# Optimization experiments

Hardware: AMD Instinct MI355X
Metric: run time of the kernel (lower is better)

The kernel has to match this reference:

```python
import jax, jax.numpy as jnp
import numpy as np

IMG_H, IMG_W = 256, 704  # full image shape (img_metas['img_shape'])
EPS = 1e-5
B, N_CAM, D_REF, C_CH = 1, 6, 1, 256
HF, WF = 32, 88
DD = 64
BEV_H = BEV_W = 128
Q = BEV_H * BEV_W


def inverse_sigmoid(x, eps=1e-5):
    x = jnp.clip(x, 0.0, 1.0)
    return jnp.log(jnp.clip(x, eps) / jnp.clip(1.0 - x, eps))


def grid_sample_2d(feat, grid):
    # feat [N,C,H,W], grid [N,Hg,Wg,2] (x,y in [-1,1]); bilinear, zeros padding, align_corners=False
    Nn, C, H, W = feat.shape
    x = (grid[..., 0] + 1.0) * 0.5 * W - 0.5
    y = (grid[..., 1] + 1.0) * 0.5 * H - 0.5
    x0 = jnp.floor(x)
    y0 = jnp.floor(y)
    wx = x - x0
    wy = y - y0
    x0 = x0.astype(jnp.int32)
    y0 = y0.astype(jnp.int32)

    def gather(ix, iy):
        valid = (ix >= 0) & (ix < W) & (iy >= 0) & (iy < H)
        ixc = jnp.clip(ix, 0, W - 1)
        iyc = jnp.clip(iy, 0, H - 1)
        v = jax.vmap(lambda f, jx, jy: f[:, jy, jx])(feat, ixc, iyc)  # [N,C,Hg,Wg]
        return v * valid[:, None].astype(feat.dtype)

    return (gather(x0, y0) * ((1 - wx) * (1 - wy))[:, None]
            + gather(x0 + 1, y0) * (wx * (1 - wy))[:, None]
            + gather(x0, y0 + 1) * ((1 - wx) * wy)[:, None]
            + gather(x0 + 1, y0 + 1) * (wx * wy)[:, None])


def grid_sample_3d(vol, grid):
    # vol [N,C,D,H,W], grid [N,Dg,Hg,Wg,3] (x,y,z); trilinear, zeros padding, align_corners=False
    Nn, C, D, H, W = vol.shape
    x = (grid[..., 0] + 1.0) * 0.5 * W - 0.5
    y = (grid[..., 1] + 1.0) * 0.5 * H - 0.5
    z = (grid[..., 2] + 1.0) * 0.5 * D - 0.5
    x0 = jnp.floor(x); y0 = jnp.floor(y); z0 = jnp.floor(z)
    wx = x - x0; wy = y - y0; wz = z - z0
    x0 = x0.astype(jnp.int32); y0 = y0.astype(jnp.int32); z0 = z0.astype(jnp.int32)

    def gather(ix, iy, iz):
        valid = (ix >= 0) & (ix < W) & (iy >= 0) & (iy < H) & (iz >= 0) & (iz < D)
        ixc = jnp.clip(ix, 0, W - 1)
        iyc = jnp.clip(iy, 0, H - 1)
        izc = jnp.clip(iz, 0, D - 1)
        v = jax.vmap(lambda f, jx, jy, jz: f[:, jz, jy, jx])(vol, ixc, iyc, izc)
        return v * valid[:, None].astype(vol.dtype)

    return (gather(x0, y0, z0) * ((1 - wx) * (1 - wy) * (1 - wz))[:, None]
            + gather(x0 + 1, y0, z0) * (wx * (1 - wy) * (1 - wz))[:, None]
            + gather(x0, y0 + 1, z0) * ((1 - wx) * wy * (1 - wz))[:, None]
            + gather(x0 + 1, y0 + 1, z0) * (wx * wy * (1 - wz))[:, None]
            + gather(x0, y0, z0 + 1) * ((1 - wx) * (1 - wy) * wz)[:, None]
            + gather(x0 + 1, y0, z0 + 1) * (wx * (1 - wy) * wz)[:, None]
            + gather(x0, y0 + 1, z0 + 1) * ((1 - wx) * wy * wz)[:, None]
            + gather(x0 + 1, y0 + 1, z0 + 1) * (wx * wy * wz)[:, None])


def setup_inputs() -> dict:
    key = jax.random.key(0)
    ks = jax.random.split(key, 12)
    feat = jax.random.normal(ks[0], (B * N_CAM, C_CH, HF, WF), jnp.float32)
    bev_queries = jax.random.normal(ks[1], (B, Q, C_CH), jnp.float32)
    bev_pos = jax.random.normal(ks[2], (B, Q, C_CH), jnp.float32)
    reference_points = jax.random.uniform(ks[3], (B, D_REF, Q, 3), jnp.float32)
    pc_range = jnp.array([-51.2, -51.2, -5.0, 51.2, 51.2, 3.0], jnp.float32)
    # semi-realistic lidar->image projection matrices: intrinsics * axis-swap * yaw per camera
    f, cx, cy = 500.0, IMG_W / 2.0, IMG_H / 2.0
    K = np.array([[f, 0, cx, 0], [0, f, cy, 0], [0, 0, 1, 0], [0, 0, 0, 1]], np.float32)
    A = np.array([[0, -1, 0, 0], [0, 0, -1, 0], [1, 0, 0, 0], [0, 0, 0, 1]], np.float32)
    mats = []
    for i in range(N_CAM):
        th = 2.0 * np.pi * i / N_CAM
        c, s = np.cos(th), np.sin(th)
        R = np.array([[c, s, 0, 0], [-s, c, 0, 0], [0, 0, 1, 0], [0, 0, 0, 1]], np.float32)
        mats.append(K @ A @ R)
    lidar_to_img = jnp.asarray(np.stack(mats))[None]  # [1,N,4,4]
    depth_prob = jax.random.uniform(ks[4], (B * N_CAM, DD, HF, WF), jnp.float32)
    sc = 0.02
    return {
        'feat': feat, 'bev_queries': bev_queries, 'bev_pos': bev_pos,
        'reference_points': reference_points, 'pc_range': pc_range,
        'lidar_to_img': lidar_to_img, 'depth_prob': depth_prob,
        'w_pos': jax.random.normal(ks[5], (C_CH, 1), jnp.float32) * sc,
        'b_pos': jnp.zeros((1,), jnp.float32),
        'w_img': jax.random.normal(ks[6], (C_CH, N_CAM * 2), jnp.float32) * sc,
        'b_img': jnp.zeros((N_CAM * 2,), jnp.float32),
        'w_att': jax.random.normal(ks[7], (C_CH, N_CAM), jnp.float32) * sc,
        'b_att': jnp.zeros((N_CAM,), jnp.float32),
        'conv_w': jax.random.normal(ks[8], (C_CH, C_CH, 3, 3), jnp.float32) * sc,
        'conv_b': jnp.zeros((C_CH,), jnp.float32),
        'bn_gamma': jnp.ones((C_CH,), jnp.float32),
        'bn_beta': jnp.zeros((C_CH,), jnp.float32),
        'bn_mean': jnp.zeros((C_CH,), jnp.float32),
        'bn_var': jnp.ones((C_CH,), jnp.float32),
        'se_w': jax.random.normal(ks[9], (C_CH, C_CH), jnp.float32) * sc,
        'se_b': jnp.zeros((C_CH,), jnp.float32),
        'cbam_w': jax.random.normal(ks[10], (1, 2, 7, 7), jnp.float32) * 0.05,
        'cbam_b': jnp.zeros((1,), jnp.float32),
        'bev_h': BEV_H, 'bev_w': BEV_W,
    }


def reference(feat, bev_queries, bev_pos, reference_points, pc_range, lidar_to_img, depth_prob,
              w_pos, b_pos, w_img, b_img, w_att, b_att, conv_w, conv_b,
              bn_gamma, bn_beta, bn_mean, bn_var, se_w, se_b, cbam_w, cbam_b, bev_h, bev_w):
    Bq, Qn = bev_queries.shape[:2]
    D = reference_points.shape[1]
    N = lidar_to_img.shape[1]
    BN, C, Hf, Wf = feat.shape
    q = bev_queries + bev_pos
    pos_offset = q @ w_pos + b_pos  # [B,Q,1] (only_use_height)
    z = jax.nn.sigmoid(inverse_sigmoid(reference_points[..., 2:3]) + pos_offset[:, None])
    rp = jnp.concatenate([reference_points[..., :2], z], axis=-1)  # [B,D,Q,3]
    attn = (q @ w_att + b_att).reshape(Bq, 1, Qn, N, 1)
    img_off = q @ w_img + b_img  # [B,Q,2N]
    # unnormalize to lidar coords; apply_3d_transformation == identity (no aug)
    pts = rp * (pc_range[3:] - pc_range[:3]) + pc_range[:3]
    pts4 = jnp.concatenate([pts, jnp.ones_like(pts[..., :1])], axis=-1)  # [B,D,Q,4]
    cam = jnp.einsum('bnij,bdqj->dbnqi', lidar_to_img, pts4)  # [D,B,N,Q,4]
    ref_depth = cam[..., 2:3]
    mask = ref_depth > EPS
    xy = cam[..., :2] / jnp.maximum(cam[..., 2:3], EPS)
    xy = xy / jnp.array([IMG_W, IMG_H], dtype=xy.dtype)
    xy = (xy - 0.5) * 2.0
    mask = mask & (xy[..., 0:1] > -1.0) & (xy[..., 0:1] < 1.0) & (xy[..., 1:2] > -1.0) & (xy[..., 1:2] < 1.0)
    Dd = depth_prob.shape[1]
    ref_depth = (ref_depth / Dd - 0.5) * 2.0
    mask = mask & (ref_depth > -1.0) & (ref_depth < 1.0)
    bev_mask = jnp.transpose(mask, (1, 4, 3, 2, 0)).astype(feat.dtype)  # [B,1,Q,N,D]
    off = img_off.reshape(Bq, Qn, N, 2).transpose(0, 2, 1, 3)[None] / jnp.array([Wf, Hf], dtype=feat.dtype)
    xy = xy + off  # [D,B,N,Q,2]
    grid = xy.transpose(1, 2, 3, 0, 4).reshape(BN, Qn, D, 2)
    sampled = grid_sample_2d(feat, grid).reshape(Bq, N, C, Qn, D).transpose(0, 2, 3, 1, 4)  # [B,C,Q,N,D]
    grid3 = jnp.concatenate([xy, ref_depth], axis=-1).transpose(1, 2, 3, 0, 4).reshape(BN, 1, Qn, D, 3)
    dp = grid_sample_3d(depth_prob[:, None], grid3).reshape(Bq, N, 1, Qn, D).transpose(0, 2, 3, 1, 4)
    bev_mask = jnp.nan_to_num(dp) * bev_mask
    w = jax.nn.sigmoid(attn) * jnp.nan_to_num(bev_mask)
    agg = (jnp.nan_to_num(sampled) * w)[..., 0].sum(-1)  # [B,C,Q] (D==1)
    x = agg.reshape(Bq, C, bev_h, bev_w)
    dn = ('NCHW', 'OIHW', 'NCHW')
    x = jax.lax.conv_general_dilated(x, conv_w, (1, 1), ((1, 1), (1, 1)), dimension_numbers=dn) + conv_b[None, :, None, None]
    x = (x - bn_mean[None, :, None, None]) * (bn_gamma / jnp.sqrt(bn_var + 1e-5))[None, :, None, None] + bn_beta[None, :, None, None]
    x = jax.nn.relu(x)
    s = x.mean(axis=(2, 3))  # SE: global avg pool + 1x1 conv + sigmoid
    x = x * jax.nn.sigmoid(s @ se_w.T + se_b)[:, :, None, None]
    a = jnp.concatenate([x.max(axis=1, keepdims=True), x.mean(axis=1, keepdims=True)], axis=1)  # CBAM spatial
    a = jax.lax.conv_general_dilated(a, cbam_w, (1, 1), ((3, 3), (3, 3)), dimension_numbers=dn) + cbam_b[None, :, None, None]
    x = x * jax.nn.sigmoid(a)
    out = x.reshape(Bq, C, bev_h * bev_w).transpose(0, 2, 1)
    return out, rp
```

## Files before the change

### kernel.cpp

```cpp
#include <hip/hip_runtime.h>
#include <math.h>

#define QN   16384
#define CCH  256
#define NCAM 6
#define HFD  32
#define WFD  88
#define DDD  64
#define BEVH 128
#define BEVW 128
#define IMGW 704.0f
#define IMGH 256.0f
#define EPSV 1e-5f

typedef __attribute__((ext_vector_type(8))) short bf8_t;
typedef __attribute__((ext_vector_type(8))) unsigned short us8;
typedef __attribute__((ext_vector_type(4))) unsigned short us4;
typedef __attribute__((ext_vector_type(4))) float f4_t;

__device__ __forceinline__ float sigmoidf_(float x){ return 1.0f/(1.0f+__expf(-x)); }

__device__ __forceinline__ unsigned short f2bf(float f){
    unsigned int b = __float_as_uint(f);
    b += 0x7FFFu + ((b >> 16) & 1u);
    return (unsigned short)(b >> 16);
}
__device__ __forceinline__ float bf2f(unsigned short u){
    return __uint_as_float(((unsigned int)u) << 16);
}

#define GLD16(gp_, lp_) __builtin_amdgcn_global_load_lds( \
    (const __attribute__((address_space(1))) unsigned int*)(gp_), \
    (__attribute__((address_space(3))) unsigned int*)(lp_), 16, 0, 0)

__global__ __launch_bounds__(256) void k_prep(const float* __restrict__ feat, unsigned short* __restrict__ feat_tH,
                                              const float* __restrict__ cw, unsigned short* __restrict__ wtH,
                                              const float* __restrict__ se_w, float* __restrict__ se_wT,
                                              float* __restrict__ ssum){
    int b = blockIdx.x;
    if (b < 4224){
        __shared__ float tile[32][33];
        int n   = b / 704;
        int rem = b - n*704;
        int cb  = (rem / 88) * 32;
        int pb  = (rem % 88) * 32;
        int tx = threadIdx.x & 31, ty = threadIdx.x >> 5;
        for (int r = ty; r < 32; r += 8)
            tile[r][tx] = feat[(size_t)(n*256 + cb + r)*2816 + pb + tx];
        __syncthreads();
        for (int r = ty; r < 32; r += 8)
            feat_tH[(size_t)(n*2816 + pb + r)*256 + cb + tx] = f2bf(tile[tx][r]);
    } else if (b < 6528){
        int b2 = b - 4224;
        if (b2 == 0) ssum[threadIdx.x] = 0.f;
        int idx = b2*256 + threadIdx.x;
        int ci = idx & 255;
        int co = (idx >> 8) & 255;
        int kk = idx >> 16;
        int kh = kk/3, kw = kk - kh*3;
        int chunk = ci >> 6, ciin = ci & 63;
        size_t dst = ((((size_t)(kh*4 + chunk)*3 + kw)*256 + co) << 6) + ciin;
        wtH[dst] = f2bf(cw[(size_t)(co*256 + ci)*9 + kk]);
    } else {
        __shared__ float tile[32][33];
        int tb = b - 6528;
        int rb_ = (tb >> 3) * 32;
        int cb_ = (tb & 7) * 32;
        int tx = threadIdx.x & 31, ty = threadIdx.x >> 5;
        for (int r = ty; r < 32; r += 8)
            tile[r][tx] = se_w[(size_t)(rb_ + r)*256 + cb_ + tx];
        __syncthreads();
        for (int r = ty; r < 32; r += 8)
            se_wT[(size_t)(cb_ + r)*256 + rb_ + tx] = tile[tx][r];
    }
}

__global__ __launch_bounds__(256) void k_proj(
    const float* __restrict__ bq, const float* __restrict__ bpos,
    const float* __restrict__ refp,
    const float* __restrict__ w_pos, const float* __restrict__ b_pos,
    const float* __restrict__ w_img, const float* __restrict__ w_att,
    float* __restrict__ Sg, float* __restrict__ out_rp)
{
    __shared__ float wlf[19][260];
    __shared__ unsigned short Aq[64][264];
    __shared__ float sl[64][20];
    int tid = threadIdx.x;
    int lane = tid & 63, wid = tid >> 6;
    int l15 = lane & 15, quad = lane >> 4;
    int q0 = blockIdx.x * 64;

    wlf[0][tid] = w_pos[tid];
    #pragma unroll
    for (int r = 0; r < 6; r++){
        int idx = r*256 + tid;
        int c = idx / 6, j = idx - 6*c;
        wlf[1 + j][c] = w_att[idx];
    }
    #pragma unroll
    for (int r = 0; r < 12; r++){
        int idx = r*256 + tid;
        int c = idx / 12, j = idx - 12*c;
        wlf[7 + j][c] = w_img[idx];
    }
    #pragma unroll
    for (int r = 0; r < 16; r++){
        int row = r*4 + wid;
        int cc  = lane * 4;
        float4 a = *(const float4*)(bq   + (size_t)(q0+row)*CCH + cc);
        float4 b = *(const float4*)(bpos + (size_t)(q0+row)*CCH + cc);
        us4 o;
        o.x = f2bf(a.x+b.x); o.y = f2bf(a.y+b.y); o.z = f2bf(a.z+b.z); o.w = f2bf(a.w+b.w);
        *(us4*)&Aq[row][cc] = o;
    }
    __syncthreads();

    f4_t acc0 = (f4_t){0.f,0.f,0.f,0.f};
    f4_t acc1 = (f4_t){0.f,0.f,0.f,0.f};
    #pragma unroll
    for (int kc = 0; kc < 8; kc++){
        bf8_t af = *(bf8_t*)&Aq[wid*16 + l15][kc*32 + quad*8];
        bf8_t b0, b1;
        {
            const float* wr = &wlf[l15][kc*32 + quad*8];
            float4 w0 = *(const float4*)wr;
            float4 w1 = *(const float4*)(wr + 4);
            b0[0]=(short)f2bf(w0.x); b0[1]=(short)f2bf(w0.y); b0[2]=(short)f2bf(w0.z); b0[3]=(short)f2bf(w0.w);
            b0[4]=(short)f2bf(w1.x); b0[5]=(short)f2bf(w1.y); b0[6]=(short)f2bf(w1.z); b0[7]=(short)f2bf(w1.w);
        }
        if (l15 < 3){
            const float* wr = &wlf[16 + l15][kc*32 + quad*8];
            float4 w0 = *(const float4*)wr;
            float4 w1 = *(const float4*)(wr + 4);
            b1[0]=(short)f2bf(w0.x); b1[1]=(short)f2bf(w0.y); b1[2]=(short)f2bf(w0.z); b1[3]=(short)f2bf(w0.w);
            b1[4]=(short)f2bf(w1.x); b1[5]=(short)f2bf(w1.y); b1[6]=(short)f2bf(w1.z); b1[7]=(short)f2bf(w1.w);
        } else {
            b1 = (bf8_t){0,0,0,0,0,0,0,0};
        }
        acc0 = __builtin_amdgcn_mfma_f32_16x16x32_bf16(af, b0, acc0, 0, 0, 0);
        acc1 = __builtin_amdgcn_mfma_f32_16x16x32_bf16(af, b1, acc1, 0, 0, 0);
    }
    #pragma unroll
    for (int r = 0; r < 4; r++){
        int qq = wid*16 + quad*4 + r;
        sl[qq][l15] = acc0[r];
        if (l15 < 3) sl[qq][16 + l15] = acc1[r];
    }
    __syncthreads();

    if (tid < 64){
        int q = q0 + tid;
        float pos_off = sl[tid][0] + b_pos[0];
        float rx = refp[q*3+0], ry = refp[q*3+1], rz = refp[q*3+2];
        float zc_ = fminf(fmaxf(rz, 0.f), 1.f);
        float inv = logf(fmaxf(zc_, EPSV) / fmaxf(1.f - zc_, EPSV));
        float znew = sigmoidf_(inv + pos_off);
        out_rp[q*3+0] = rx; out_rp[q*3+1] = ry; out_rp[q*3+2] = znew;
        sl[tid][19] = znew;
    }
    __syncthreads();

    for (int i = tid; i < 64*20; i += 256)
        Sg[(size_t)q0*20 + i] = ((const float*)sl)[i];
}

__global__ __launch_bounds__(256) void k_geomagg(
    const float* __restrict__ refp, const float* __restrict__ pcr,
    const float* __restrict__ l2i, const float* __restrict__ dpr,
    const float* __restrict__ b_img, const float* __restrict__ b_att,
    const float* __restrict__ Sg, const unsigned short* __restrict__ feat_tH,
    unsigned short* __restrict__ aggH)
{
    __shared__ float sgl[8][20];
    __shared__ int   so_l[192];
    __shared__ float sw_l[192];
    int q0 = blockIdx.x * 8;
    int tid = threadIdx.x;
    int wid = tid >> 6, lane = tid & 63;

    if (tid < 160) ((float*)sgl)[tid] = Sg[(size_t)q0*20 + tid];
    __syncthreads();

    {
        int sub = lane >> 5;
        int n   = lane & 31;
        if (n < NCAM){
            int ql = wid*2 + sub;
            int q  = q0 + ql;
            float att  = sgl[ql][1+n] + b_att[n];
            float offx = (sgl[ql][7+2*n] + b_img[2*n])   / (float)WFD;
            float offy = (sgl[ql][8+2*n] + b_img[2*n+1]) / (float)HFD;
            float znew = sgl[ql][19];
            float rx = refp[q*3+0], ry = refp[q*3+1];
            float lo0=pcr[0], lo1=pcr[1], lo2=pcr[2];
            float hi0=pcr[3], hi1=pcr[4], hi2=pcr[5];
            float px = rx*(hi0-lo0)+lo0, py = ry*(hi1-lo1)+lo1, pz = znew*(hi2-lo2)+lo2;
            const float* M = l2i + n*16;
            float cx = M[0]*px + M[1]*py + M[2]*pz  + M[3];
            float cy = M[4]*px + M[5]*py + M[6]*pz  + M[7];
            float cz = M[8]*px + M[9]*py + M[10]*pz + M[11];
            bool m = cz > EPSV;
            float zdiv = fmaxf(cz, EPSV);
            float u = (cx/zdiv)/IMGW; u = (u - 0.5f)*2.f;
            float v = (cy/zdiv)/IMGH; v = (v - 0.5f)*2.f;
            m = m && (u > -1.f) && (u < 1.f) && (v > -1.f) && (v < 1.f);
            float rdn = (cz/(float)DDD - 0.5f)*2.f;
            m = m && (rdn > -1.f) && (rdn < 1.f);

            int base = ql*24 + n*4;
            float wq = 0.f, xs = 0.f, ys = 0.f;
            if (m){
                float u2 = u + offx, v2 = v + offy;
                xs = (u2 + 1.f)*0.5f*WFD - 0.5f;
                ys = (v2 + 1.f)*0.5f*HFD - 0.5f;
                float zs = (rdn + 1.f)*0.5f*DDD - 0.5f;
                float fx = floorf(xs), fy = floorf(ys), fz = floorf(zs);
                int x0=(int)fx, y0=(int)fy, z0=(int)fz;
                float wx = xs-fx, wy = ys-fy, wz = zs-fz;
                float dp = 0.f;
                const float* vol = dpr + (size_t)n*DDD*HFD*WFD;
                #pragma unroll
                for (int dz=0; dz<2; dz++)
                #pragma unroll
                for (int dy=0; dy<2; dy++)
                #pragma unroll
                for (int dx=0; dx<2; dx++){
                    int ix=x0+dx, iy=y0+dy, iz=z0+dz;
                    if (ix>=0 && ix<WFD && iy>=0 && iy<HFD && iz>=0 && iz<DDD){
                        float ww = (dx?wx:1.f-wx)*(dy?wy:1.f-wy)*(dz?wz:1.f-wz);
                        dp += ww * vol[(size_t)(iz*HFD+iy)*WFD + ix];
                    }
                }
                wq = sigmoidf_(att) * dp;
            }
            if (m && wq != 0.f){
                float fx = floorf(xs), fy = floorf(ys);
                int x0=(int)fx, y0=(int)fy;
                float wx = xs-fx, wy = ys-fy;
                float cwv[4] = {(1.f-wx)*(1.f-wy), wx*(1.f-wy), (1.f-wx)*wy, wx*wy};
                int xi[4] = {x0, x0+1, x0, x0+1};
                int yi[4] = {y0, y0, y0+1, y0+1};
                #pragma unroll
                for (int k=0;k<4;k++){
                    bool ok = (xi[k]>=0 && xi[k]<WFD && yi[k]>=0 && yi[k]<HFD);
                    so_l[base+k] = ok ? ((n*HFD + yi[k])*WFD + xi[k]) : 0;
                    sw_l[base+k] = ok ? wq*cwv[k] : 0.f;
                }
            } else {
                #pragma unroll
                for (int k=0;k<4;k++){ so_l[base+k] = 0; sw_l[base+k] = 0.f; }
            }
        }
    }
    __syncthreads();

    int cnt;
    {
        int half = lane >> 5, li = lane & 31;
        int ql = wid*2 + half;
        bool p = false;
        int   so_v = 0;
        float sw_v = 0.f;
        if (li < 24){
            sw_v = sw_l[ql*24 + li];
            so_v = so_l[ql*24 + li];
            p = (sw_v != 0.f);
        }
        unsigned long long m64 = __ballot(p);
        unsigned int hm = (unsigned int)(half ? (m64 >> 32) : m64);
        cnt = __popc(hm);
        int pos = __popc(hm & ((1u << li) - 1u));
        if (p){
            so_l[ql*24 + pos] = so_v;
            sw_l[ql*24 + pos] = sw_v;
        }
    }

    {
        int half = lane >> 5, li = lane & 31;
        int c8 = li * 8;
        int ql = wid*2 + half;
        float a[8] = {0.f,0.f,0.f,0.f,0.f,0.f,0.f,0.f};
        for (int k=0;k<cnt;k++){
            float w = sw_l[ql*24+k];
            us8 v = *(const us8*)(feat_tH + (size_t)so_l[ql*24+k]*CCH + c8);
            #pragma unroll
            for (int j=0;j<8;j++) a[j] += w * bf2f((unsigned short)v[j]);
        }
        us8 o;
        #pragma unroll
        for (int j=0;j<8;j++) o[j] = f2bf(a[j]);
        *(us8*)(aggH + (size_t)(q0+ql)*CCH + c8) = o;
    }
}

__global__ __launch_bounds__(256, 2) void k_conv2(const unsigned short* __restrict__ aggH,
    const unsigned short* __restrict__ wtH, const float* __restrict__ conv_b,
    const float* __restrict__ bn_g, const float* __restrict__ bn_b,
    const float* __restrict__ bn_m, const float* __restrict__ bn_v,
    float* __restrict__ xN, float* __restrict__ ssum)
{
    __shared__ unsigned short Abuf[2][128][64];
    __shared__ unsigned short Bbuf[2][3][64][64];

    int h   = blockIdx.x;
    int co0 = blockIdx.y * 64;
    int tid  = threadIdx.x;
    int lane = tid & 63, wid = tid >> 6;
    int m_q = (wid & 1) * 64;
    int n_q = (wid >> 1) * 32;
    int l15 = lane & 15, quad = lane >> 4;
    int swB = l15 & 7;

    f4_t acc[4][2];
    #pragma unroll
    for (int i=0;i<4;i++)
    #pragma unroll
    for (int j=0;j<2;j++) acc[i][j] = (f4_t){0.f,0.f,0.f,0.f};

    const us8 z8 = (us8){0,0,0,0,0,0,0,0};
    const bf8_t zf = (bf8_t){0,0,0,0,0,0,0,0};

    #define LOADA(s, bq_) { \
        int kh_ = (s) >> 2; \
        int ph_ = h + kh_ - 1; \
        if (ph_ >= 0 && ph_ < BEVH){ \
            _Pragma("unroll") \
            for (int k_=0; k_<4; k_++){ \
                int w_ = (k_*256 + tid) >> 3; \
                int sd_ = tid & 7; \
                const unsigned short* gp_ = aggH + ((size_t)(ph_*BEVW + w_)*CCH + (((s) & 3) << 6)) \
                                            + ((sd_ ^ (w_ & 7)) << 3); \
                unsigned short* lp_ = &Abuf[bq_][k_*32 + wid*8][0]; \
                GLD16(gp_, lp_); \
            } \
        } else { \
            _Pragma("unroll") \
            for (int k_=0; k_<4; k_++){ \
                int w_ = (k_*256 + tid) >> 3; \
                int sd_ = tid & 7; \
                *(us8*)&Abuf[bq_][w_][sd_*8] = z8; \
            } \
        } \
    }

    #define LOADB(s, bq_) { \
        const unsigned short* bp_ = wtH + (size_t)(s)*49152 + (size_t)co0*64; \
        int srcsw_ = (((tid & 7) ^ ((tid >> 3) & 7)) << 3); \
        _Pragma("unroll") \
        for (int kw_=0; kw_<3; kw_++){ \
            _Pragma("unroll") \
            for (int j_=0; j_<2; j_++){ \
                const unsigned short* gp_ = bp_ + kw_*16384 + (size_t)(j_*32 + (tid>>3))*64 + srcsw_; \
                unsigned short* lp_ = &Bbuf[bq_][kw_][j_*32 + wid*8][0]; \
                GLD16(gp_, lp_); \
            } \
        } \
    }

    LOADA(0, 0);
    LOADB(0, 0);
    int buf = 0;

    for (int s=0; s<12; s++){
        __syncthreads();
        if (s < 11){
            LOADA(s+1, buf^1);
            LOADB(s+1, buf^1);
        }
        #pragma unroll
        for (int ks=0; ks<2; ks++){
            #pragma unroll
            for (int kw=0; kw<3; kw++){
                bf8_t af[4], bfr[2];
                #pragma unroll
                for (int i=0;i<4;i++){
                    int aw = m_q + i*16 + l15 + kw - 1;
                    int awc = min(max(aw, 0), 127);
                    int aslot = (((ks<<2)|quad) ^ (awc & 7));
                    af[i] = *(bf8_t*)&Abuf[buf][awc][aslot*8];
                    if (kw==0 && i==0){ if (m_q==0  && l15==0)  af[i] = zf; }
                    if (kw==2 && i==3){ if (m_q==64 && l15==15) af[i] = zf; }
                }
                #pragma unroll
                for (int j=0;j<2;j++){
                    int slot = (((ks<<2) | quad) ^ swB);
                    bfr[j] = *(bf8_t*)&Bbuf[buf][kw][n_q + j*16 + l15][slot*8];
                }
                #pragma unroll
                for (int i=0;i<4;i++)
                #pragma unroll
                for (int j=0;j<2;j++)
                    acc[i][j] = __builtin_amdgcn_mfma_f32_16x16x32_bf16(af[i], bfr[j], acc[i][j], 0, 0, 0);
            }
        }
        buf ^= 1;
    }
    #undef LOADA
    #undef LOADB

    __syncthreads();
    float* sacc = (float*)&Abuf[0][0][0];
    if (tid < 64) sacc[tid] = 0.f;
    __syncthreads();

    #pragma unroll
    for (int j=0;j<2;j++){
        int col = n_q + j*16 + l15;
        int co = co0 + col;
        float sc = bn_g[co] * rsqrtf(bn_v[co] + 1e-5f);
        float sh = bn_b[co] - bn_m[co]*sc;
        float cb = conv_b[co];
        float part = 0.f;
        #pragma unroll
        for (int i=0;i<4;i++){
            #pragma unroll
            for (int r=0;r<4;r++){
                int m = m_q + i*16 + quad*4 + r;
                int p = h*BEVW + m;
                float y = fmaxf((acc[i][j][r] + cb)*sc + sh, 0.f);
                xN[(size_t)p*CCH + co] = y;
                part += y;
            }
        }
        atomicAdd(&sacc[col], part);
    }
    __syncthreads();
    if (tid < 64) atomicAdd(&ssum[co0 + tid], sacc[tid]);
}

__global__ __launch_bounds__(256) void k_maps2(const float* __restrict__ xN,
    const float* __restrict__ ssum, const float* __restrict__ se_wT, const float* __restrict__ se_b,
    float* __restrict__ scale_g, float* __restrict__ amax, float* __restrict__ amean)
{
    __shared__ float smv[256];
    __shared__ float scl[256];
    int t = threadIdx.x;
    smv[t] = ssum[t] * (1.f/16384.f);
    __syncthreads();
    float a0=0.f, a1=0.f, a2=0.f, a3=0.f;
    for (int k=0; k<256; k+=4){
        a0 += smv[k]   * se_wT[(size_t)(k  )*256 + t];
        a1 += smv[k+1] * se_wT[(size_t)(k+1)*256 + t];
        a2 += smv[k+2] * se_wT[(size_t)(k+2)*256 + t];
        a3 += smv[k+3] * se_wT[(size_t)(k+3)*256 + t];
    }
    float sv = sigmoidf_(se_b[t] + ((a0+a1)+(a2+a3)));
    scl[t] = sv;
    if (blockIdx.x == 0) scale_g[t] = sv;
    __syncthreads();

    int wid = t >> 6, lane = t & 63;
    int p0 = blockIdx.x * 64;
    float4 sc = *(const float4*)&scl[lane*4];
    for (int i=0; i<16; i++){
        int p = p0 + i*4 + wid;
        float4 v = *(const float4*)&xN[(size_t)p*CCH + lane*4];
        float a = v.x*sc.x, b = v.y*sc.y, c = v.z*sc.z, d = v.w*sc.w;
        float mx = fmaxf(fmaxf(a,b), fmaxf(c,d));
        float sm = a+b+c+d;
        #pragma unroll
        for (int off=1; off<64; off<<=1){
            mx = fmaxf(mx, __shfl_xor(mx, off, 64));
            sm += __shfl_xor(sm, off, 64);
        }
        if (lane == 0){ amax[p] = mx; amean[p] = sm*(1.f/256.f); }
    }
}

__global__ __launch_bounds__(256) void k_final2(const float* __restrict__ xN,
    const float* __restrict__ scale_g, const float* __restrict__ amax, const float* __restrict__ amean,
    const float* __restrict__ cw, const float* __restrict__ cb, float* __restrict__ out)
{
    __shared__ float am2[7][128];
    __shared__ float av2[7][128];
    __shared__ float wcb[98];
    __shared__ float scl[256];
    __shared__ float amap_l[64];

    int b = blockIdx.x;
    int h  = b >> 1;
    int w0 = (b & 1) * 64;
    int t = threadIdx.x;

    scl[t] = scale_g[t];
    if (t < 98) wcb[t] = cw[t];
    for (int idx = t; idx < 896; idx += 256){
        int r = idx >> 7, c = idx & 127;
        int ph = h + r - 3;
        bool ok = (ph >= 0 && ph < BEVH);
        am2[r][c] = ok ? amax[ph*BEVW + c] : 0.f;
        av2[r][c] = ok ? amean[ph*BEVW + c] : 0.f;
    }
    __syncthreads();

    if (t < 64){
        int px = w0 + t;
        float acc = cb[0];
        #pragma unroll
        for (int kh=0; kh<7; kh++){
            #pragma unroll
            for (int kw=0; kw<7; kw++){
                int pw = px + kw - 3;
                if (pw >= 0 && pw < BEVW)
                    acc += am2[kh][pw]*wcb[kh*7+kw] + av2[kh][pw]*wcb[49 + kh*7+kw];
            }
        }
        amap_l[t] = sigmoidf_(acc);
    }
    __syncthreads();

    int lane = t & 63, sub = t >> 6;
    int c4 = lane * 4;
    float4 sc = *(const float4*)&scl[c4];
    for (int i=0; i<16; i++){
        int pxl = sub*16 + i;
        int p = h*BEVW + w0 + pxl;
        float am = amap_l[pxl];
        float4 v = *(const float4*)&xN[(size_t)p*CCH + c4];
        float4 o;
        o.x = v.x*sc.x*am; o.y = v.y*sc.y*am; o.z = v.z*sc.z*am; o.w = v.w*sc.w*am;
        *(float4*)&out[(size_t)p*CCH + c4] = o;
    }
}

extern "C" void kernel_launch(void* const* d_in, const int* in_sizes, int n_in,
                              void* d_out, int out_size, void* d_ws, size_t ws_size,
                              hipStream_t stream) {
    const float* feat   = (const float*)d_in[0];
    const float* bq     = (const float*)d_in[1];
    const float* bpos   = (const float*)d_in[2];
    const float* refp   = (const float*)d_in[3];
    const float* pcr    = (const float*)d_in[4];
    const float* l2i    = (const float*)d_in[5];
    const float* dpr    = (const float*)d_in[6];
    const float* w_pos  = (const float*)d_in[7];
    const float* b_pos  = (const float*)d_in[8];
    const float* w_img  = (const float*)d_in[9];
    const float* b_img  = (const float*)d_in[10];
    const float* w_att  = (const float*)d_in[11];
    const float* b_att  = (const float*)d_in[12];
    const float* conv_w = (const float*)d_in[13];
    const float* conv_b = (const float*)d_in[14];
    const float* bn_g   = (const float*)d_in[15];
    const float* bn_b   = (const float*)d_in[16];
    const float* bn_m   = (const float*)d_in[17];
    const float* bn_v   = (const float*)d_in[18];
    const float* se_w   = (const float*)d_in[19];
    const float* se_b   = (const float*)d_in[20];
    const float* cbw    = (const float*)d_in[21];
    const float* cbb    = (const float*)d_in[22];
    float* out = (float*)d_out;

    float* ws = (float*)d_ws;
    size_t o = 0;
    unsigned short* feat_tH = (unsigned short*)(ws + o); o += (size_t)6*2816*128;
    unsigned short* wtH  = (unsigned short*)(ws + o); o += (size_t)9*256*128;
    unsigned short* aggH = (unsigned short*)(ws + o); o += (size_t)QN*128;
    float* xN      = ws + o;  o += (size_t)QN*256;
    float* se_wT   = ws + o;  o += (size_t)256*256;
    float* Sg      = ws + o;  o += (size_t)QN*20;
    float* ssum    = ws + o;  o += 256;
    float* scale_g = ws + o;  o += 256;
    float* amax    = ws + o;  o += QN;
    float* amean   = ws + o;  o += QN;

    k_prep<<<6592, 256, 0, stream>>>(feat, feat_tH, conv_w, wtH, se_w, se_wT, ssum);
    k_proj<<<256, 256, 0, stream>>>(bq, bpos, refp, w_pos, b_pos, w_img, w_att,
                                    Sg, out + (size_t)QN*256);
    k_geomagg<<<2048, 256, 0, stream>>>(refp, pcr, l2i, dpr, b_img, b_att,
                                        Sg, feat_tH, aggH);
    k_conv2<<<dim3(128,4), 256, 0, stream>>>(aggH, wtH, conv_b, bn_g, bn_b, bn_m, bn_v, xN, ssum);
    k_maps2<<<256, 256, 0, stream>>>(xN, ssum, se_wT, se_b, scale_g, amax, amean);
    k_final2<<<256, 256, 0, stream>>>(xN, scale_g, amax, amean, cbw, cbb, out);
}
```

Baseline: 209.4 us.

## Merge projection kernel into prep kernel and swizzle geomagg block order

```diff
diff --git a/kernel.cpp b/kernel.cpp
--- a/kernel.cpp
+++ b/kernel.cpp
@@ -36,24 +36,112 @@
 __global__ __launch_bounds__(256) void k_prep(const float* __restrict__ feat, unsigned short* __restrict__ feat_tH,
                                               const float* __restrict__ cw, unsigned short* __restrict__ wtH,
                                               const float* __restrict__ se_w, float* __restrict__ se_wT,
-                                              float* __restrict__ ssum){
+                                              float* __restrict__ ssum,
+                                              const float* __restrict__ bq, const float* __restrict__ bpos,
+                                              const float* __restrict__ refp,
+                                              const float* __restrict__ w_pos, const float* __restrict__ b_pos,
+                                              const float* __restrict__ w_img, const float* __restrict__ w_att,
+                                              float* __restrict__ Sg, float* __restrict__ out_rp){
+    __shared__ float wlf[19][260];
+    __shared__ float sl[64][20];
+    __shared__ float tile[32][33];
     int b = blockIdx.x;
-    if (b < 4224){
-        __shared__ float tile[32][33];
-        int n   = b / 704;
-        int rem = b - n*704;
+    int tid = threadIdx.x;
+
+    if (b < 256){
+        int lane = tid & 63, wid = tid >> 6;
+        int l15 = lane & 15, quad = lane >> 4;
+        int q0 = b * 64;
+
+        wlf[0][tid] = w_pos[tid];
+        #pragma unroll
+        for (int r = 0; r < 6; r++){
+            int idx = r*256 + tid;
+            int c = idx / 6, j = idx - 6*c;
+            wlf[1 + j][c] = w_att[idx];
+        }
+        #pragma unroll
+        for (int r = 0; r < 12; r++){
+            int idx = r*256 + tid;
+            int c = idx / 12, j = idx - 12*c;
+            wlf[7 + j][c] = w_img[idx];
+        }
+        __syncthreads();
+
+        f4_t acc0 = (f4_t){0.f,0.f,0.f,0.f};
+        f4_t acc1 = (f4_t){0.f,0.f,0.f,0.f};
+        const float* qrow = bq   + (size_t)(q0 + wid*16 + l15)*CCH;
+        const float* prow = bpos + (size_t)(q0 + wid*16 + l15)*CCH;
+        #pragma unroll
+        for (int kc = 0; kc < 8; kc++){
+            int cc = kc*32 + quad*8;
+            float4 a0 = *(const float4*)(qrow + cc);
+            float4 a1 = *(const float4*)(qrow + cc + 4);
+            float4 p0 = *(const float4*)(prow + cc);
+            float4 p1 = *(const float4*)(prow + cc + 4);
+            bf8_t af;
+            af[0]=(short)f2bf(a0.x+p0.x); af[1]=(short)f2bf(a0.y+p0.y);
+            af[2]=(short)f2bf(a0.z+p0.z); af[3]=(short)f2bf(a0.w+p0.w);
+            af[4]=(short)f2bf(a1.x+p1.x); af[5]=(short)f2bf(a1.y+p1.y);
+            af[6]=(short)f2bf(a1.z+p1.z); af[7]=(short)f2bf(a1.w+p1.w);
+            bf8_t b0, b1;
+            {
+                const float* wr = &wlf[l15][cc];
+                float4 w0 = *(const float4*)wr;
+                float4 w1 = *(const float4*)(wr + 4);
+                b0[0]=(short)f2bf(w0.x); b0[1]=(short)f2bf(w0.y); b0[2]=(short)f2bf(w0.z); b0[3]=(short)f2bf(w0.w);
+                b0[4]=(short)f2bf(w1.x); b0[5]=(short)f2bf(w1.y); b0[6]=(short)f2bf(w1.z); b0[7]=(short)f2bf(w1.w);
+            }
+            if (l15 < 3){
+                const float* wr = &wlf[16 + l15][cc];
+                float4 w0 = *(const float4*)wr;
+                float4 w1 = *(const float4*)(wr + 4);
+                b1[0]=(short)f2bf(w0.x); b1[1]=(short)f2bf(w0.y); b1[2]=(short)f2bf(w0.z); b1[3]=(short)f2bf(w0.w);
+                b1[4]=(short)f2bf(w1.x); b1[5]=(short)f2bf(w1.y); b1[6]=(short)f2bf(w1.z); b1[7]=(short)f2bf(w1.w);
+            } else {
+                b1 = (bf8_t){0,0,0,0,0,0,0,0};
+            }
+            acc0 = __builtin_amdgcn_mfma_f32_16x16x32_bf16(af, b0, acc0, 0, 0, 0);
+            acc1 = __builtin_amdgcn_mfma_f32_16x16x32_bf16(af, b1, acc1, 0, 0, 0);
+        }
+        #pragma unroll
+        for (int r = 0; r < 4; r++){
+            int qq = wid*16 + quad*4 + r;
+            sl[qq][l15] = acc0[r];
+            if (l15 < 3) sl[qq][16 + l15] = acc1[r];
+        }
+        __syncthreads();
+
+        if (tid < 64){
+            int q = q0 + tid;
+            float pos_off = sl[tid][0] + b_pos[0];
+            float rx = refp[q*3+0], ry = refp[q*3+1], rz = refp[q*3+2];
+            float zc_ = fminf(fmaxf(rz, 0.f), 1.f);
+            float inv = logf(fmaxf(zc_, EPSV) / fmaxf(1.f - zc_, EPSV));
+            float znew = sigmoidf_(inv + pos_off);
+            out_rp[q*3+0] = rx; out_rp[q*3+1] = ry; out_rp[q*3+2] = znew;
+            sl[tid][19] = znew;
+        }
+        __syncthreads();
+
+        for (int i = tid; i < 64*20; i += 256)
+            Sg[(size_t)q0*20 + i] = ((const float*)sl)[i];
+    } else if (b < 4480){
+        int bb = b - 256;
+        int n   = bb / 704;
+        int rem = bb - n*704;
         int cb  = (rem / 88) * 32;
         int pb  = (rem % 88) * 32;
-        int tx = threadIdx.x & 31, ty = threadIdx.x >> 5;
+        int tx = tid & 31, ty = tid >> 5;
         for (int r = ty; r < 32; r += 8)
             tile[r][tx] = feat[(size_t)(n*256 + cb + r)*2816 + pb + tx];
         __syncthreads();
         for (int r = ty; r < 32; r += 8)
             feat_tH[(size_t)(n*2816 + pb + r)*256 + cb + tx] = f2bf(tile[tx][r]);
-    } else if (b < 6528){
-        int b2 = b - 4224;
-        if (b2 == 0) ssum[threadIdx.x] = 0.f;
-        int idx = b2*256 + threadIdx.x;
+    } else if (b < 6784){
+        int b2 = b - 4480;
+        if (b2 == 0) ssum[tid] = 0.f;
+        int idx = b2*256 + tid;
         int ci = idx & 255;
         int co = (idx >> 8) & 255;
         int kk = idx >> 16;
@@ -62,106 +150,16 @@
         size_t dst = ((((size_t)(kh*4 + chunk)*3 + kw)*256 + co) << 6) + ciin;
         wtH[dst] = f2bf(cw[(size_t)(co*256 + ci)*9 + kk]);
     } else {
-        __shared__ float tile[32][33];
-        int tb = b - 6528;
+        int tb = b - 6784;
         int rb_ = (tb >> 3) * 32;
         int cb_ = (tb & 7) * 32;
-        int tx = threadIdx.x & 31, ty = threadIdx.x >> 5;
+        int tx = tid & 31, ty = tid >> 5;
         for (int r = ty; r < 32; r += 8)
             tile[r][tx] = se_w[(size_t)(rb_ + r)*256 + cb_ + tx];
         __syncthreads();
         for (int r = ty; r < 32; r += 8)
             se_wT[(size_t)(cb_ + r)*256 + rb_ + tx] = tile[tx][r];
     }
-}
-
-__global__ __launch_bounds__(256) void k_proj(
-    const float* __restrict__ bq, const float* __restrict__ bpos,
-    const float* __restrict__ refp,
-    const float* __restrict__ w_pos, const float* __restrict__ b_pos,
-    const float* __restrict__ w_img, const float* __restrict__ w_att,
-    float* __restrict__ Sg, float* __restrict__ out_rp)
-{
-    __shared__ float wlf[19][260];
-    __shared__ unsigned short Aq[64][264];
-    __shared__ float sl[64][20];
-    int tid = threadIdx.x;
-    int lane = tid & 63, wid = tid >> 6;
-    int l15 = lane & 15, quad = lane >> 4;
-    int q0 = blockIdx.x * 64;
-
-    wlf[0][tid] = w_pos[tid];
-    #pragma unroll
-    for (int r = 0; r < 6; r++){
-        int idx = r*256 + tid;
-        int c = idx / 6, j = idx - 6*c;
-        wlf[1 + j][c] = w_att[idx];
-    }
-    #pragma unroll
-    for (int r = 0; r < 12; r++){
-        int idx = r*256 + tid;
-        int c = idx / 12, j = idx - 12*c;
-        wlf[7 + j][c] = w_img[idx];
-    }
-    #pragma unroll
-    for (int r = 0; r < 16; r++){
-        int row = r*4 + wid;
-        int cc  = lane * 4;
-        float4 a = *(const float4*)(bq   + (size_t)(q0+row)*CCH + cc);
-        float4 b = *(const float4*)(bpos + (size_t)(q0+row)*CCH + cc);
-        us4 o;
-        o.x = f2bf(a.x+b.x); o.y = f2bf(a.y+b.y); o.z = f2bf(a.z+b.z); o.w = f2bf(a.w+b.w);
-        *(us4*)&Aq[row][cc] = o;
-    }
-    __syncthreads();
-
-    f4_t acc0 = (f4_t){0.f,0.f,0.f,0.f};
-    f4_t acc1 = (f4_t){0.f,0.f,0.f,0.f};
-    #pragma unroll
-    for (int kc = 0; kc < 8; kc++){
-        bf8_t af = *(bf8_t*)&Aq[wid*16 + l15][kc*32 + quad*8];
-        bf8_t b0, b1;
-        {
-            const float* wr = &wlf[l15][kc*32 + quad*8];
-            float4 w0 = *(const float4*)wr;
-            float4 w1 = *(const float4*)(wr + 4);
-            b0[0]=(short)f2bf(w0.x); b0[1]=(short)f2bf(w0.y); b0[2]=(short)f2bf(w0.z); b0[3]=(short)f2bf(w0.w);
-            b0[4]=(short)f2bf(w1.x); b0[5]=(short)f2bf(w1.y); b0[6]=(short)f2bf(w1.z); b0[7]=(short)f2bf(w1.w);
-        }
-        if (l15 < 3){
-            const float* wr = &wlf[16 + l15][kc*32 + quad*8];
-            float4 w0 = *(const float4*)wr;
-            float4 w1 = *(const float4*)(wr + 4);
-            b1[0]=(short)f2bf(w0.x); b1[1]=(short)f2bf(w0.y); b1[2]=(short)f2bf(w0.z); b1[3]=(short)f2bf(w0.w);
-            b1[4]=(short)f2bf(w1.x); b1[5]=(short)f2bf(w1.y); b1[6]=(short)f2bf(w1.z); b1[7]=(short)f2bf(w1.w);
-        } else {
-            b1 = (bf8_t){0,0,0,0,0,0,0,0};
-        }
-        acc0 = __builtin_amdgcn_mfma_f32_16x16x32_bf16(af, b0, acc0, 0, 0, 0);
-        acc1 = __builtin_amdgcn_mfma_f32_16x16x32_bf16(af, b1, acc1, 0, 0, 0);
-    }
-    #pragma unroll
-    for (int r = 0; r < 4; r++){
-        int qq = wid*16 + quad*4 + r;
-        sl[qq][l15] = acc0[r];
-        if (l15 < 3) sl[qq][16 + l15] = acc1[r];
-    }
-    __syncthreads();
-
-    if (tid < 64){
-        int q = q0 + tid;
-        float pos_off = sl[tid][0] + b_pos[0];
-        float rx = refp[q*3+0], ry = refp[q*3+1], rz = refp[q*3+2];
-        float zc_ = fminf(fmaxf(rz, 0.f), 1.f);
-        float inv = logf(fmaxf(zc_, EPSV) / fmaxf(1.f - zc_, EPSV));
-        float znew = sigmoidf_(inv + pos_off);
-        out_rp[q*3+0] = rx; out_rp[q*3+1] = ry; out_rp[q*3+2] = znew;
-        sl[tid][19] = znew;
-    }
-    __syncthreads();
-
-    for (int i = tid; i < 64*20; i += 256)
-        Sg[(size_t)q0*20 + i] = ((const float*)sl)[i];
 }
 
 __global__ __launch_bounds__(256) void k_geomagg(
@@ -174,7 +172,9 @@
     __shared__ float sgl[8][20];
     __shared__ int   so_l[192];
     __shared__ float sw_l[192];
-    int q0 = blockIdx.x * 8;
+    int bid = blockIdx.x;
+    int swz = (bid & 7) * 256 + (bid >> 3);
+    int q0 = swz * 8;
     int tid = threadIdx.x;
     int wid = tid >> 6, lane = tid & 63;
 
@@ -565,9 +565,9 @@
     float* amax    = ws + o;  o += QN;
     float* amean   = ws + o;  o += QN;
 
-    k_prep<<<6592, 256, 0, stream>>>(feat, feat_tH, conv_w, wtH, se_w, se_wT, ssum);
-    k_proj<<<256, 256, 0, stream>>>(bq, bpos, refp, w_pos, b_pos, w_img, w_att,
-                                    Sg, out + (size_t)QN*256);
+    k_prep<<<6848, 256, 0, stream>>>(feat, feat_tH, conv_w, wtH, se_w, se_wT, ssum,
+                                     bq, bpos, refp, w_pos, b_pos, w_img, w_att,
+                                     Sg, out + (size_t)QN*256);
     k_geomagg<<<2048, 256, 0, stream>>>(refp, pcr, l2i, dpr, b_img, b_att,
                                         Sg, feat_tH, aggH);
     k_conv2<<<dim3(128,4), 256, 0, stream>>>(aggH, wtH, conv_b, bn_g, bn_b, bn_m, bn_v, xN, ssum);
```

Result: no change. 207.5 us (-0.9%).
